# Performance work log

Hardware: AMD Instinct MI355X
Metric: run time of the kernel (lower is better)

## Reference

```python
import jax, jax.numpy as jnp
import numpy as np

N = 100000
E = 800000
D_IN = 128
D_HID = 128
D_EMB = 128
D_OUT = 2


def setup_inputs() -> dict:
    key = jax.random.key(0)
    ks = jax.random.split(key, 16)
    x = jax.random.normal(ks[0], (N, D_IN), dtype=jnp.float32)
    edge_index = jax.random.randint(ks[1], (2, E), 0, N, dtype=jnp.int64)

    def lin(k, d_out, d_in, scale):
        return jax.random.normal(k, (d_out, d_in), dtype=jnp.float32) * scale

    s1 = 1.0 / np.sqrt(D_IN)
    s2 = 1.0 / np.sqrt(D_HID)
    s3 = 1.0 / np.sqrt(D_EMB)
    return {
        "x": x,
        "edge_index": edge_index,
        # layer 1: in -> hidden  (lin_l has bias, lin_r no bias, as in PyG SAGEConv)
        "Wl1": lin(ks[2], D_HID, D_IN, s1), "bl1": jnp.zeros((D_HID,), jnp.float32),
        "Wr1": lin(ks[3], D_HID, D_IN, s1),
        # layer 2: hidden -> hidden
        "Wl2": lin(ks[4], D_HID, D_HID, s2), "bl2": jnp.zeros((D_HID,), jnp.float32),
        "Wr2": lin(ks[5], D_HID, D_HID, s2),
        # layer 3: hidden -> embedding
        "Wl3": lin(ks[6], D_EMB, D_HID, s2), "bl3": jnp.zeros((D_EMB,), jnp.float32),
        "Wr3": lin(ks[7], D_EMB, D_HID, s2),
        # output head: embedding -> output (bias)
        "Wo": lin(ks[8], D_OUT, D_EMB, s3), "bo": jnp.zeros((D_OUT,), jnp.float32),
    }


def _sage_conv(x, src, dst, Wl, bl, Wr):
    # mean-aggregate neighbor (source) features onto destination nodes
    msg = x[src]                                             # [E, d]
    agg = jax.ops.segment_sum(msg, dst, num_segments=N)      # [N, d]
    deg = jax.ops.segment_sum(jnp.ones((src.shape[0],), x.dtype), dst, num_segments=N)
    agg = agg / jnp.maximum(deg, 1.0)[:, None]
    # out = lin_l(agg) + lin_r(x)
    return agg @ Wl.T + bl + x @ Wr.T


def reference(x, edge_index, Wl1, bl1, Wr1, Wl2, bl2, Wr2, Wl3, bl3, Wr3, Wo, bo):
    src, dst = edge_index[0], edge_index[1]
    h = jax.nn.relu(_sage_conv(x, src, dst, Wl1, bl1, Wr1))   # dropout is identity in eval
    h = jax.nn.relu(_sage_conv(h, src, dst, Wl2, bl2, Wr2))
    h = _sage_conv(h, src, dst, Wl3, bl3, Wr3)                # no relu on last conv
    return h @ Wo.T + bo                                      # [N, D_OUT]
```

## Files before the change

### kernel.cpp

```cpp
#include <hip/hip_runtime.h>
#include <stdint.h>

typedef unsigned int u32;
typedef unsigned short u16;
typedef __bf16 bf16x8 __attribute__((ext_vector_type(8)));
typedef float floatx16 __attribute__((ext_vector_type(16)));
typedef u32 u32x4 __attribute__((ext_vector_type(4)));
typedef float floatx4 __attribute__((ext_vector_type(4)));

__device__ __forceinline__ u16 f2b(float f) {
    u32 u = __builtin_bit_cast(u32, f);
    u32 r = u + 0x7FFFu + ((u >> 16) & 1u);
    return (u16)(r >> 16);
}
__device__ __forceinline__ float lo2f(u32 u) { return __builtin_bit_cast(float, u << 16); }
__device__ __forceinline__ float hi2f(u32 u) { return __builtin_bit_cast(float, u & 0xFFFF0000u); }


__device__ __forceinline__ void self_detect(const int* ei, const u32* xw, int& is64, int& isbf) {
    int lane = threadIdx.x & 63;
    int v = ei ? ei[2 * lane + 1] : 0;
    unsigned long long b1 = __ballot(v == 0);
    u32 w = xw ? xw[lane] : 0;
    u32 e = (w >> 7) & 0xFF;
    int plaus = (e == 0) || (e >= 90 && e <= 140);
    unsigned long long b2 = __ballot(plaus);
    is64 = (b1 == ~0ULL) ? 1 : 0;
    isbf = (b2 == ~0ULL) ? 1 : 0;
}

__device__ __forceinline__ int load_id(const int* __restrict__ ei, int is64, size_t pos, int N) {
    int v = is64 ? ei[2 * pos] : ei[pos];
    unsigned u = (unsigned)v;
    if (u >= (unsigned)N) u = 0;
    return (int)u;
}

__device__ __forceinline__ float load_f(const void* __restrict__ p, int isbf, size_t i) {
    if (isbf) {
        u16 s = ((const u16*)p)[i];
        return __builtin_bit_cast(float, ((u32)s) << 16);
    }
    return ((const float*)p)[i];
}


#define CH 4096
#define CAPB 3072

__global__ __launch_bounds__(1024) void front_kernel(
    const void* __restrict__ xraw, const int* __restrict__ ei, int E, int N, int cvb,
    u32* __restrict__ xb, int* __restrict__ gcur, u32* __restrict__ csrbkt,
    const void* Wl1, const void* Wr1, const void* Wl2, const void* Wr2,
    const void* Wl3, const void* Wr3, const void* b1, const void* b2,
    const void* b3, const void* Wo, const void* bo,
    u16* __restrict__ Wcp, float* __restrict__ smalls) {
    __shared__ int lhist[1024], loff[1024], lcur[1024], gofs[1024], wsum[16];
    __shared__ u32 ebuf[CH];
    __shared__ u16 ebkt[CH];
    int blk = blockIdx.x;
    int t = threadIdx.x;

    if (blk < cvb) {
        int is64, isbf;
        self_detect(nullptr, (const u32*)xraw, is64, isbf);
        int i = blk * 1024 + t;
        int count4 = N * 16;
        if (i >= count4) return;
        if (isbf) {
            ((u32x4*)xb)[i] = ((const u32x4*)xraw)[i];
        } else {
            const floatx4* f4 = (const floatx4*)xraw;
            floatx4 f0 = f4[2 * i], f1 = f4[2 * i + 1];
            u32x4 o;
            o.x = (u32)f2b(f0.x) | ((u32)f2b(f0.y) << 16);
            o.y = (u32)f2b(f0.z) | ((u32)f2b(f0.w) << 16);
            o.z = (u32)f2b(f1.x) | ((u32)f2b(f1.y) << 16);
            o.w = (u32)f2b(f1.z) | ((u32)f2b(f1.w) << 16);
            ((u32x4*)xb)[i] = o;
        }
        return;
    }
    if (blk < cvb + 12) {
        int is64, isbf;
        self_detect(nullptr, (const u32*)xraw, is64, isbf);
        int tg = (blk - cvb) * 1024 + t;
        int l = tg >> 12;
        int tt = tg & 4095;
        const void* Wl = (l == 0) ? Wl1 : (l == 1) ? Wl2 : Wl3;
        const void* Wr = (l == 0) ? Wr1 : (l == 1) ? Wr2 : Wr3;
        u16* Wout = Wcp + (size_t)l * 32768;
        int lane = tt & 63;
        int jt = (tt >> 6) & 3;
        int s = tt >> 8;
        int n = lane & 31;
        int q = lane >> 5;
        int j = jt * 32 + n;
#pragma unroll
        for (int jj = 0; jj < 8; ++jj) {
            int k = s * 16 + q * 8 + jj;
            float v = (k < 128) ? load_f(Wl, isbf, (size_t)j * 128 + k)
                                : load_f(Wr, isbf, (size_t)j * 128 + (k - 128));
            Wout[tt * 8 + jj] = f2b(v);
        }
        return;
    }
    if (blk == cvb + 12) {
        int is64, isbf;
        self_detect(nullptr, (const u32*)xraw, is64, isbf);
        if (t < 642) {
            float v;
            if (t < 128) v = load_f(b1, isbf, t);
            else if (t < 256) v = load_f(b2, isbf, t - 128);
            else if (t < 384) v = load_f(b3, isbf, t - 256);
            else if (t < 640) v = load_f(Wo, isbf, t - 384);
            else v = load_f(bo, isbf, t - 640);
            smalls[t] = v;
        }
        return;
    }

    int is64, isbf;
    self_detect(ei, nullptr, is64, isbf);
    int cbase = (blk - (cvb + 13)) * CH;
    int cn = E - cbase;
    if (cn > CH) cn = CH;
    lhist[t] = 0;
    __syncthreads();
    int mysrc[4], myb[4], mydl[4];
#pragma unroll
    for (int k = 0; k < 4; ++k) {
        int i = t + k * 1024;
        myb[k] = -1;
        if (i < cn) {
            int e = cbase + i;
            int s = load_id(ei, is64, (size_t)e, N);
            int d = load_id(ei, is64, (size_t)E + e, N);
            mysrc[k] = s;
            mydl[k] = d & 255;
            myb[k] = d >> 8;
            atomicAdd(&lhist[myb[k]], 1);
        }
    }
    __syncthreads();
    int lane = t & 63, wid = t >> 6;
    int v = lhist[t];
    int inc = v;
#pragma unroll
    for (int off = 1; off < 64; off <<= 1) {
        int o = __shfl_up(inc, off);
        if (lane >= off) inc += o;
    }
    if (lane == 63) wsum[wid] = inc;
    __syncthreads();
    int wpre = 0;
    for (int w = 0; w < wid; ++w) wpre += wsum[w];
    int excl = wpre + inc - v;
    loff[t] = excl;
    lcur[t] = excl;
    if (v > 0) gofs[t] = atomicAdd(&gcur[t], v);
    __syncthreads();
#pragma unroll
    for (int k = 0; k < 4; ++k) {
        if (myb[k] >= 0) {
            int pos = atomicAdd(&lcur[myb[k]], 1);
            ebuf[pos] = (u32)mysrc[k] | ((u32)mydl[k] << 24);
            ebkt[pos] = (u16)myb[k];
        }
    }
    __syncthreads();
#pragma unroll
    for (int k = 0; k < 4; ++k) {
        int i = t + k * 1024;
        if (i < cn) {
            int bb = ebkt[i];
            int local = gofs[bb] + (i - loff[bb]);
            if (local < CAPB) csrbkt[(size_t)bb * CAPB + local] = ebuf[i];
        }
    }
}

__global__ void csr_build_kernel(const u32* __restrict__ csrbkt, const int* __restrict__ gcur,
                                 int N, int* __restrict__ gtot,
                                 int* __restrict__ offs, int* __restrict__ cnt,
                                 int* __restrict__ csr) {
    __shared__ int lh[256], lcur[256], wsum[4];
    __shared__ int sbase;
    __shared__ u32 sbuf[CAPB];
    int t = threadIdx.x;
    int b = blockIdx.x;
    int cb = gcur[b];
    if (cb > CAPB) cb = CAPB;
    const u32* bsrc = csrbkt + (size_t)b * CAPB;
    int d0 = b << 8;
    lh[t] = 0;
    __syncthreads();
    for (int i = t; i < cb; i += 256) atomicAdd(&lh[bsrc[i] >> 24], 1);
    __syncthreads();
    int lane = t & 63, wid = t >> 6;
    int v = lh[t];
    int inc = v;
#pragma unroll
    for (int off = 1; off < 64; off <<= 1) {
        int o = __shfl_up(inc, off);
        if (lane >= off) inc += o;
    }
    if (lane == 63) wsum[wid] = inc;
    __syncthreads();
    int wpre = 0;
    for (int w = 0; w < wid; ++w) wpre += wsum[w];
    int excl = wpre + inc - v;
    lcur[t] = excl;
    if (t == 0) sbase = atomicAdd(gtot, cb);
    __syncthreads();
    int base = sbase;
    int d = d0 + t;
    if (d < N) {
        offs[d] = base + excl;
        cnt[d] = v;
    }
    for (int i = t; i < cb; i += 256) {
        u32 e = bsrc[i];
        int pos = atomicAdd(&lcur[e >> 24], 1);
        sbuf[pos] = e & 0xFFFFFFu;
    }
    __syncthreads();
    for (int i = t; i < cb; i += 256) csr[base + i] = (int)sbuf[i];
}


__global__ void agg_kernel(const u32* __restrict__ F2, const int* __restrict__ offs,
                           const int* __restrict__ cnt, const int* __restrict__ csr,
                           u32* __restrict__ Aout, int N, int tstride) {
    int sub = blockIdx.x / tstride;
    int tile = blockIdx.x % tstride;
    int w = threadIdx.x >> 6;
    int lane = threadIdx.x & 63;
    int nd0 = tile * 128 + sub * 16 + w * 4;
    if (nd0 >= N) return;
    int nd1 = nd0 + 4 < N ? nd0 + 4 : N;
    for (int nd = nd0; nd < nd1; ++nd) {
        int start = offs[nd];
        int num = cnt[nd];
        float a0 = 0.f, a1 = 0.f;
        int i = 0;
        for (; i + 8 <= num; i += 8) {
            int s0 = csr[start + i + 0], s1 = csr[start + i + 1];
            int s2 = csr[start + i + 2], s3 = csr[start + i + 3];
            int s4 = csr[start + i + 4], s5 = csr[start + i + 5];
            int s6 = csr[start + i + 6], s7 = csr[start + i + 7];
            u32 u0 = F2[(size_t)s0 * 64 + lane];
            u32 u1 = F2[(size_t)s1 * 64 + lane];
            u32 u2 = F2[(size_t)s2 * 64 + lane];
            u32 u3 = F2[(size_t)s3 * 64 + lane];
            u32 u4 = F2[(size_t)s4 * 64 + lane];
            u32 u5 = F2[(size_t)s5 * 64 + lane];
            u32 u6 = F2[(size_t)s6 * 64 + lane];
            u32 u7 = F2[(size_t)s7 * 64 + lane];
            a0 += lo2f(u0) + lo2f(u1) + lo2f(u2) + lo2f(u3) +
                  lo2f(u4) + lo2f(u5) + lo2f(u6) + lo2f(u7);
            a1 += hi2f(u0) + hi2f(u1) + hi2f(u2) + hi2f(u3) +
                  hi2f(u4) + hi2f(u5) + hi2f(u6) + hi2f(u7);
        }
        for (; i + 4 <= num; i += 4) {
            int s0 = csr[start + i + 0], s1 = csr[start + i + 1];
            int s2 = csr[start + i + 2], s3 = csr[start + i + 3];
            u32 u0 = F2[(size_t)s0 * 64 + lane];
            u32 u1 = F2[(size_t)s1 * 64 + lane];
            u32 u2 = F2[(size_t)s2 * 64 + lane];
            u32 u3 = F2[(size_t)s3 * 64 + lane];
            a0 += lo2f(u0) + lo2f(u1) + lo2f(u2) + lo2f(u3);
            a1 += hi2f(u0) + hi2f(u1) + hi2f(u2) + hi2f(u3);
        }
        for (; i < num; ++i) {
            u32 u = F2[(size_t)csr[start + i] * 64 + lane];
            a0 += lo2f(u);
            a1 += hi2f(u);
        }
        float sc = 1.0f / (float)(num > 1 ? num : 1);
        a0 *= sc;
        a1 *= sc;
        Aout[(size_t)nd * 64 + lane] = (u32)f2b(a0) | ((u32)f2b(a1) << 16);
    }
}


__global__ void gemm_kernel(const u32* __restrict__ aggb, u32* Fio,
                            const u16* __restrict__ Wcp, const float* __restrict__ biasf,
                            int N, int relu, const float* __restrict__ headw,
                            const u32* __restrict__ xw, void* __restrict__ outp) {
    int tid = threadIdx.x;
    int w = tid >> 6;
    int lane = tid & 63;
    int nbase = blockIdx.x * 128;
    int n = lane & 31;
    int q = lane >> 5;
    int rowl = w * 32 + n;
    int node = nbase + rowl;
    int nodeC = (node < N) ? node : (N - 1);
    const u32* aRow = aggb + (size_t)nodeC * 64 + q * 4;
    const u32* fRow = Fio + (size_t)nodeC * 64 + q * 4;

    floatx16 acc0 = 0.0f, acc1 = 0.0f, acc2 = 0.0f, acc3 = 0.0f;

#pragma unroll
    for (int s = 0; s < 16; ++s) {
        const u32* ap = (s < 8) ? (aRow + (size_t)s * 8) : (fRow + (size_t)(s - 8) * 8);
        bf16x8 a = *reinterpret_cast<const bf16x8*>(ap);
        const u16* bp = Wcp + (size_t)((s * 4) * 64 + lane) * 8;
        bf16x8 b0 = *reinterpret_cast<const bf16x8*>(bp);
        bf16x8 b1 = *reinterpret_cast<const bf16x8*>(bp + 64 * 8);
        bf16x8 b2 = *reinterpret_cast<const bf16x8*>(bp + 2 * 64 * 8);
        bf16x8 b3 = *reinterpret_cast<const bf16x8*>(bp + 3 * 64 * 8);
        acc0 = __builtin_amdgcn_mfma_f32_32x32x16_bf16(a, b0, acc0, 0, 0, 0);
        acc1 = __builtin_amdgcn_mfma_f32_32x32x16_bf16(a, b1, acc1, 0, 0, 0);
        acc2 = __builtin_amdgcn_mfma_f32_32x32x16_bf16(a, b2, acc2, 0, 0, 0);
        acc3 = __builtin_amdgcn_mfma_f32_32x32x16_bf16(a, b3, acc3, 0, 0, 0);
    }

    int mbase = nbase + w * 32;
    floatx16 accs[4] = {acc0, acc1, acc2, acc3};

    if (outp == nullptr) {
#pragma unroll
        for (int jt = 0; jt < 4; ++jt) {
            int j0 = jt * 32 + n;
            float bf = biasf[j0];
#pragma unroll
            for (int r = 0; r < 16; ++r) {
                int row = (r & 3) + 8 * (r >> 2) + 4 * q;
                int nodeS = mbase + row;
                if (nodeS < N) {
                    float v = accs[jt][r] + bf;
                    if (relu) v = fmaxf(v, 0.0f);
                    u16* dst16 = (u16*)&Fio[(size_t)nodeS * 64];
                    dst16[j0] = f2b(v);
                }
            }
        }
    } else {
        int is64, isbf;
        self_detect(nullptr, xw, is64, isbf);
#pragma unroll
        for (int r = 0; r < 16; ++r) {
            float p0 = 0.f, p1 = 0.f;
#pragma unroll
            for (int jt = 0; jt < 4; ++jt) {
                int j = jt * 32 + n;
                float v = accs[jt][r] + biasf[j];
                p0 += v * headw[j];
                p1 += v * headw[128 + j];
            }
#pragma unroll
            for (int off = 16; off > 0; off >>= 1) {
                p0 += __shfl_xor(p0, off);
                p1 += __shfl_xor(p1, off);
            }
            if (n == 0) {
                int row = (r & 3) + 8 * (r >> 2) + 4 * q;
                int nodeS = mbase + row;
                if (nodeS < N) {
                    float o0 = p0 + headw[256];
                    float o1 = p1 + headw[257];
                    if (isbf)
                        ((u32*)outp)[nodeS] = (u32)f2b(o0) | ((u32)f2b(o1) << 16);
                    else
                        ((float2*)outp)[nodeS] = make_float2(o0, o1);
                }
            }
        }
    }
}

extern "C" void kernel_launch(void* const* d_in, const int* in_sizes, int n_in,
                              void* d_out, int out_size, void* d_ws, size_t ws_size,
                              hipStream_t stream) {
    const int N = in_sizes[0] / 128;
    const int E = in_sizes[1] / 2;

    const void* x = d_in[0];
    const int* ei = (const int*)d_in[1];
    const void* Wl[3] = {d_in[2], d_in[5], d_in[8]};
    const void* bl[3] = {d_in[3], d_in[6], d_in[9]};
    const void* Wr[3] = {d_in[4], d_in[7], d_in[10]};
    const void* Wo = d_in[11];
    const void* bo = d_in[12];

    char* p = (char*)d_ws;
    auto alloc = [&](size_t bytes) -> char* {
        char* r = p;
        p += (bytes + 255) & ~(size_t)255;
        return r;
    };
    int* offs = (int*)alloc((size_t)N * 4);
    int* cnt = (int*)alloc((size_t)N * 4);
    float* smalls = (float*)alloc(642 * 4);
    int* gcur = (int*)alloc(1025 * 4);
    int* csr = (int*)alloc((size_t)E * 4);
    u16* Wcp = (u16*)alloc((size_t)3 * 4096 * 8 * 2);
    u32* xb = (u32*)alloc((size_t)N * 64 * 4);
    u32* aggb = (u32*)alloc((size_t)N * 64 * 4);
    u32* csrbkt = aggb;
    int* gtot = gcur + 1024;
    (void)ws_size;

    const int NB = (N + 255) / 256;
    const int cvb = (N * 16 + 1023) / 1024;
    const int sb = (E + CH - 1) / CH;
    const int gb = (N + 127) / 128;
    const int tstride = (gb + 7) & ~7;
    const int ab = 8 * tstride;

    hipMemsetAsync(gcur, 0, 1025 * 4, stream);
    front_kernel<<<cvb + 13 + sb, 1024, 0, stream>>>(
        x, ei, E, N, cvb, xb, gcur, csrbkt,
        Wl[0], Wr[0], Wl[1], Wr[1], Wl[2], Wr[2],
        bl[0], bl[1], bl[2], Wo, bo, Wcp, smalls);
    csr_build_kernel<<<NB, 256, 0, stream>>>(csrbkt, gcur, N, gtot, offs, cnt, csr);

    agg_kernel<<<ab, 256, 0, stream>>>(xb, offs, cnt, csr, aggb, N, tstride);
    gemm_kernel<<<gb, 256, 0, stream>>>(aggb, xb, Wcp, smalls, N, 1, nullptr, nullptr, nullptr);
    agg_kernel<<<ab, 256, 0, stream>>>(xb, offs, cnt, csr, aggb, N, tstride);
    gemm_kernel<<<gb, 256, 0, stream>>>(aggb, xb, Wcp + 32768, smalls + 128, N, 1, nullptr, nullptr, nullptr);
    agg_kernel<<<ab, 256, 0, stream>>>(xb, offs, cnt, csr, aggb, N, tstride);
    gemm_kernel<<<gb, 256, 0, stream>>>(aggb, xb, Wcp + 65536, smalls + 256, N, 0,
                                        smalls + 384, (const u32*)x, d_out);
}
```

Before: 340.7 us.

## Restructure neighbor aggregation to process four nodes concurrently with half-wave edge split

The aggregation kernel now has each wave gather all four of its destination nodes at once instead of looping over them one by one. Each half-wave handles alternating edges and each lane loads 8-byte vectors, and the two halves are combined with a cross-half shuffle. The goal is more independent gather loads in flight per wave to hide latency on the irregular neighbor reads. In exchange, nodes with fewer edges than the longest of the four do padded loads that are masked out, register use rises, and the csr and source indices are clamped to stay in bounds.

```diff
diff --git a/kernel.cpp b/kernel.cpp
--- a/kernel.cpp
+++ b/kernel.cpp
@@ -231,56 +231,84 @@
 
 __global__ void agg_kernel(const u32* __restrict__ F2, const int* __restrict__ offs,
                            const int* __restrict__ cnt, const int* __restrict__ csr,
-                           u32* __restrict__ Aout, int N, int tstride) {
+                           u32* __restrict__ Aout, int N, int E, int tstride) {
     int sub = blockIdx.x / tstride;
     int tile = blockIdx.x % tstride;
     int w = threadIdx.x >> 6;
     int lane = threadIdx.x & 63;
+    int li = lane & 31;
+    int half = lane >> 5;
     int nd0 = tile * 128 + sub * 16 + w * 4;
     if (nd0 >= N) return;
-    int nd1 = nd0 + 4 < N ? nd0 + 4 : N;
-    for (int nd = nd0; nd < nd1; ++nd) {
-        int start = offs[nd];
-        int num = cnt[nd];
-        float a0 = 0.f, a1 = 0.f;
-        int i = 0;
-        for (; i + 8 <= num; i += 8) {
-            int s0 = csr[start + i + 0], s1 = csr[start + i + 1];
-            int s2 = csr[start + i + 2], s3 = csr[start + i + 3];
-            int s4 = csr[start + i + 4], s5 = csr[start + i + 5];
-            int s6 = csr[start + i + 6], s7 = csr[start + i + 7];
-            u32 u0 = F2[(size_t)s0 * 64 + lane];
-            u32 u1 = F2[(size_t)s1 * 64 + lane];
-            u32 u2 = F2[(size_t)s2 * 64 + lane];
-            u32 u3 = F2[(size_t)s3 * 64 + lane];
-            u32 u4 = F2[(size_t)s4 * 64 + lane];
-            u32 u5 = F2[(size_t)s5 * 64 + lane];
-            u32 u6 = F2[(size_t)s6 * 64 + lane];
-            u32 u7 = F2[(size_t)s7 * 64 + lane];
-            a0 += lo2f(u0) + lo2f(u1) + lo2f(u2) + lo2f(u3) +
-                  lo2f(u4) + lo2f(u5) + lo2f(u6) + lo2f(u7);
-            a1 += hi2f(u0) + hi2f(u1) + hi2f(u2) + hi2f(u3) +
-                  hi2f(u4) + hi2f(u5) + hi2f(u6) + hi2f(u7);
-        }
-        for (; i + 4 <= num; i += 4) {
-            int s0 = csr[start + i + 0], s1 = csr[start + i + 1];
-            int s2 = csr[start + i + 2], s3 = csr[start + i + 3];
-            u32 u0 = F2[(size_t)s0 * 64 + lane];
-            u32 u1 = F2[(size_t)s1 * 64 + lane];
-            u32 u2 = F2[(size_t)s2 * 64 + lane];
-            u32 u3 = F2[(size_t)s3 * 64 + lane];
-            a0 += lo2f(u0) + lo2f(u1) + lo2f(u2) + lo2f(u3);
-            a1 += hi2f(u0) + hi2f(u1) + hi2f(u2) + hi2f(u3);
-        }
-        for (; i < num; ++i) {
-            u32 u = F2[(size_t)csr[start + i] * 64 + lane];
-            a0 += lo2f(u);
-            a1 += hi2f(u);
-        }
-        float sc = 1.0f / (float)(num > 1 ? num : 1);
-        a0 *= sc;
-        a1 *= sc;
-        Aout[(size_t)nd * 64 + lane] = (u32)f2b(a0) | ((u32)f2b(a1) << 16);
+
+    int st[4], ct[4];
+#pragma unroll
+    for (int j = 0; j < 4; ++j) {
+        int nd = nd0 + j;
+        st[j] = (nd < N) ? offs[nd] : 0;
+        ct[j] = (nd < N) ? cnt[nd] : 0;
+    }
+
+    float acc[4][4];
+#pragma unroll
+    for (int j = 0; j < 4; ++j)
+#pragma unroll
+        for (int f = 0; f < 4; ++f) acc[j][f] = 0.f;
+
+    int maxct = max(max(ct[0], ct[1]), max(ct[2], ct[3]));
+    int Em1 = E - 1;
+    int pos = 0;
+    while (pos < maxct) {
+        u32 da[4][4], db[4][4];
+        int vld[4][4];
+#pragma unroll
+        for (int j = 0; j < 4; ++j) {
+#pragma unroll
+            for (int k = 0; k < 4; ++k) {
+                int e = pos + k * 2 + half;
+                int v = (e < ct[j]) ? 1 : 0;
+                vld[j][k] = v;
+                int idx = st[j] + (v ? e : 0);
+                if (idx > Em1) idx = Em1;
+                u32 s = (u32)csr[idx] & 0xFFFFFFu;
+                if (s >= (u32)N) s = 0;
+                uint2 u = *reinterpret_cast<const uint2*>(F2 + ((size_t)s * 64 + li * 2));
+                da[j][k] = u.x;
+                db[j][k] = u.y;
+            }
+        }
+#pragma unroll
+        for (int j = 0; j < 4; ++j) {
+#pragma unroll
+            for (int k = 0; k < 4; ++k) {
+                u32 a = vld[j][k] ? da[j][k] : 0u;
+                u32 b = vld[j][k] ? db[j][k] : 0u;
+                acc[j][0] += lo2f(a);
+                acc[j][1] += hi2f(a);
+                acc[j][2] += lo2f(b);
+                acc[j][3] += hi2f(b);
+            }
+        }
+        pos += 8;
+    }
+
+#pragma unroll
+    for (int j = 0; j < 4; ++j)
+#pragma unroll
+        for (int f = 0; f < 4; ++f) acc[j][f] += __shfl_xor(acc[j][f], 32);
+
+    if (half == 0) {
+#pragma unroll
+        for (int j = 0; j < 4; ++j) {
+            int nd = nd0 + j;
+            if (nd < N) {
+                float sc = 1.0f / (float)(ct[j] > 1 ? ct[j] : 1);
+                u32 o0 = (u32)f2b(acc[j][0] * sc) | ((u32)f2b(acc[j][1] * sc) << 16);
+                u32 o1 = (u32)f2b(acc[j][2] * sc) | ((u32)f2b(acc[j][3] * sc) << 16);
+                *reinterpret_cast<uint2*>(Aout + ((size_t)nd * 64 + li * 2)) =
+                    make_uint2(o0, o1);
+            }
+        }
     }
 }
 
@@ -418,11 +446,11 @@
         bl[0], bl[1], bl[2], Wo, bo, Wcp, smalls);
     csr_build_kernel<<<NB, 256, 0, stream>>>(csrbkt, gcur, N, gtot, offs, cnt, csr);
 
-    agg_kernel<<<ab, 256, 0, stream>>>(xb, offs, cnt, csr, aggb, N, tstride);
+    agg_kernel<<<ab, 256, 0, stream>>>(xb, offs, cnt, csr, aggb, N, E, tstride);
     gemm_kernel<<<gb, 256, 0, stream>>>(aggb, xb, Wcp, smalls, N, 1, nullptr, nullptr, nullptr);
-    agg_kernel<<<ab, 256, 0, stream>>>(xb, offs, cnt, csr, aggb, N, tstride);
+    agg_kernel<<<ab, 256, 0, stream>>>(xb, offs, cnt, csr, aggb, N, E, tstride);
     gemm_kernel<<<gb, 256, 0, stream>>>(aggb, xb, Wcp + 32768, smalls + 128, N, 1, nullptr, nullptr, nullptr);
-    agg_kernel<<<ab, 256, 0, stream>>>(xb, offs, cnt, csr, aggb, N, tstride);
+    agg_kernel<<<ab, 256, 0, stream>>>(xb, offs, cnt, csr, aggb, N, E, tstride);
     gemm_kernel<<<gb, 256, 0, stream>>>(aggb, xb, Wcp + 65536, smalls + 256, N, 0,
                                         smalls + 384, (const u32*)x, d_out);
 }
```

New measurement: 333.3 us. 2.2% less time.
